# Kernel optimization log

Measured on AMD Instinct MI355X. Metric: run time of the kernel, lower is better.

Reference implementation:

```python
import jax, jax.numpy as jnp
import numpy as np

MAX_COLLISIONS = 8
EPS = 1e-6


def _interval(p, dd):
    """Moller interval on the intersection line. p, dd: [..., 3] projections and
    signed plane distances of one triangle's vertices. Returns (lo, hi)."""
    p0, p1, p2 = p[..., 0], p[..., 1], p[..., 2]
    d0, d1, d2 = dd[..., 0], dd[..., 1], dd[..., 2]

    def seg(pa, da, pb, db, pc, dc):
        # vertex a is isolated on one side of the other triangle's plane
        den1 = db - da
        den2 = dc - da
        den1 = jnp.where(jnp.abs(den1) < 1e-12, 1e-12, den1)
        den2 = jnp.where(jnp.abs(den2) < 1e-12, 1e-12, den2)
        t1 = pb + (pa - pb) * db / den1
        t2 = pc + (pa - pc) * dc / den2
        return jnp.minimum(t1, t2), jnp.maximum(t1, t2)

    lo2, hi2 = seg(p2, d2, p0, d0, p1, d1)  # verts 0,1 on same side -> 2 isolated
    lo1, hi1 = seg(p1, d1, p0, d0, p2, d2)  # verts 0,2 on same side -> 1 isolated
    lo0, hi0 = seg(p0, d0, p1, d1, p2, d2)  # verts 1,2 on same side -> 0 isolated
    c2 = d0 * d1 > 0
    c1 = jnp.logical_and(~c2, d0 * d2 > 0)
    lo = jnp.where(c2, lo2, jnp.where(c1, lo1, lo0))
    hi = jnp.where(c2, hi2, jnp.where(c1, hi1, hi0))
    return lo, hi


def _collide_mask(tris):
    """tris: [B, F, 3, 3]. Returns bool [B, F, F] (upper-triangular) of
    triangle-triangle intersections (Moller test, coplanar pairs ignored,
    pairs sharing a vertex excluded -- same policy as the BVH CUDA kernel)."""
    B, F = tris.shape[0], tris.shape[1]
    v0 = tris[..., 0, :]
    N = jnp.cross(tris[..., 1, :] - v0, tris[..., 2, :] - v0)  # [B,F,3]
    d = -jnp.einsum('bfc,bfc->bf', N, v0)

    # du[b,f,g,k]: signed distance of triangle g's vertex k to plane of triangle f
    du = jnp.einsum('bfc,bgkc->bfgk', N, tris) + d[:, :, None, None]
    # dv[b,f,g,k]: signed distance of triangle f's vertex k to plane of triangle g
    dv = jnp.einsum('bgc,bfkc->bfgk', N, tris) + d[:, None, :, None]
    du = jnp.where(jnp.abs(du) < EPS, 0.0, du)
    dv = jnp.where(jnp.abs(dv) < EPS, 0.0, dv)

    no_u = (du[..., 0] * du[..., 1] > 0) & (du[..., 0] * du[..., 2] > 0)
    no_v = (dv[..., 0] * dv[..., 1] > 0) & (dv[..., 0] * dv[..., 2] > 0)
    coplanar = jnp.all(du == 0.0, axis=-1)

    # direction of the plane-plane intersection line; project onto dominant axis
    D = jnp.cross(N[:, :, None, :], N[:, None, :, :])  # [B,F,F,3]
    axis = jnp.argmax(jnp.abs(D), axis=-1)             # [B,F,F]
    oh = jax.nn.one_hot(axis, 3, dtype=tris.dtype)     # [B,F,F,3]
    vp = jnp.einsum('bfkc,bfgc->bfgk', tris, oh)  # proj of tri f's verts
    up = jnp.einsum('bgkc,bfgc->bfgk', tris, oh)  # proj of tri g's verts

    lo1, hi1 = _interval(vp, dv)
    lo2, hi2 = _interval(up, du)
    overlap = jnp.maximum(lo1, lo2) <= jnp.minimum(hi1, hi2)

    collide = (~no_u) & (~no_v) & (~coplanar) & overlap

    # exclude pairs sharing a vertex (exact coordinate match), and i >= j
    shared = jnp.any(
        jnp.all(tris[:, :, None, :, None, :] == tris[:, None, :, None, :, :], axis=-1),
        axis=(-1, -2))
    upper = jnp.triu(jnp.ones((F, F), dtype=bool), k=1)
    return collide & (~shared) & upper


def setup_inputs() -> dict:
    key = jax.random.key(0)
    triangles = jax.random.normal(key, (2, 1024, 3, 3), dtype=jnp.float32)
    return {"triangles": triangles}


def reference(triangles):
    B, F = triangles.shape[0], triangles.shape[1]
    K = F * MAX_COLLISIONS  # fixed-size output slot count, as in the CUDA kernel
    mask = _collide_mask(triangles)             # [B,F,F] bool
    flat = mask.reshape(B, F * F)
    # stable sort: colliding pairs (True) first, in (i,j) lexicographic order
    order = jnp.argsort(~flat, axis=1)[:, :K]   # [B,K]
    valid = jnp.take_along_axis(flat, order, axis=1)
    pairs = jnp.stack([order // F, order % F], axis=-1)  # [B,K,2]
    pairs = jnp.where(valid[..., None], pairs, -1)
    return pairs.astype(jnp.int32)
```

## Files before the change

### kernel.cpp

```cpp
#include <hip/hip_runtime.h>
#include <hip/hip_bf16.h>

#pragma clang fp contract(off)

#define F 1024
#define MAXC 8
#define K (F * MAXC)
#define WORDS_PER_ROW 16
#define WORDS_PER_BATCH (F * WORDS_PER_ROW)
#define EPS 1e-6f
#define IT 8

#define WS_MASK(ws) ((unsigned long long*)(ws))

__device__ __forceinline__ void tri_plane(const float* T, float N[3], float& d) {
    float e1x = T[3] - T[0], e1y = T[4] - T[1], e1z = T[5] - T[2];
    float e2x = T[6] - T[0], e2y = T[7] - T[1], e2z = T[8] - T[2];
    N[0] = e1y * e2z - e1z * e2y;
    N[1] = e1z * e2x - e1x * e2z;
    N[2] = e1x * e2y - e1y * e2x;
    d = -((N[0] * T[0] + N[1] * T[1]) + N[2] * T[2]);
}

__device__ __forceinline__ void interval_sel(
    float p0, float p1, float p2, float d0, float d1, float d2,
    float& lo, float& hi) {
    bool c2 = (d0 * d1 > 0.0f);
    bool c1 = (!c2) && (d0 * d2 > 0.0f);
    bool c21 = c2 || c1;
    float pa = c2 ? p2 : (c1 ? p1 : p0);
    float da = c2 ? d2 : (c1 ? d1 : d0);
    float pb = c21 ? p0 : p1;
    float db = c21 ? d0 : d1;
    float pc = c2 ? p1 : p2;
    float dc = c2 ? d1 : d2;
    float den1 = db - da;
    float den2 = dc - da;
    if (fabsf(den1) < 1e-12f) den1 = 1e-12f;
    if (fabsf(den2) < 1e-12f) den2 = 1e-12f;
    float t1 = pb + (pa - pb) * db / den1;
    float t2 = pc + (pa - pc) * dc / den2;
    lo = fminf(t1, t2);
    hi = fmaxf(t1, t2);
}

__global__ __launch_bounds__(256) void pairs_kernel(
    const float* __restrict__ tris, unsigned long long* __restrict__ mask) {
    const int b = blockIdx.z;
    const int i0 = blockIdx.y * IT;
    const int j0 = blockIdx.x * 256;
    const int tid = threadIdx.x;
    const float* tb = tris + (size_t)b * F * 9;
    unsigned long long* mb = mask + (size_t)b * WORDS_PER_BATCH;
    const int word0 = j0 >> 6;

    if (j0 + 255 <= i0) {
        if (tid < IT * 4) {
            int r = tid >> 2, w = tid & 3;
            mb[(i0 + r) * WORDS_PER_ROW + word0 + w] = 0ull;
        }
        return;
    }

    __shared__ float sh[256 * 9];
    __shared__ float shPl[IT][4];
    __shared__ float shTf[IT][9];
    {
        const float4* src = (const float4*)(tb + j0 * 9);
        float4* dst = (float4*)sh;
        for (int idx = tid; idx < 576; idx += 256)
            dst[idx] = src[idx];
    }
    if (tid < IT) {
        const float* T = tb + (i0 + tid) * 9;
        float N[3], d;
        tri_plane(T, N, d);
        shPl[tid][0] = N[0]; shPl[tid][1] = N[1];
        shPl[tid][2] = N[2]; shPl[tid][3] = d;
        #pragma unroll
        for (int k = 0; k < 9; k++) shTf[tid][k] = T[k];
    }
    __syncthreads();

    const int j = j0 + tid;
    const int lane = tid & 63;
    const int wv = tid >> 6;
    const int jmax = j0 + (wv << 6) + 63;

    float g0 = sh[tid * 9 + 0], g1 = sh[tid * 9 + 1], g2 = sh[tid * 9 + 2];
    float g3 = sh[tid * 9 + 3], g4 = sh[tid * 9 + 4], g5 = sh[tid * 9 + 5];
    float g6 = sh[tid * 9 + 6], g7 = sh[tid * 9 + 7], g8 = sh[tid * 9 + 8];
    float Ng0, Ng1, Ng2, dg;
    {
        float e1x = g3 - g0, e1y = g4 - g1, e1z = g5 - g2;
        float e2x = g6 - g0, e2y = g7 - g1, e2z = g8 - g2;
        Ng0 = e1y * e2z - e1z * e2y;
        Ng1 = e1z * e2x - e1x * e2z;
        Ng2 = e1x * e2y - e1y * e2x;
        dg = -((Ng0 * g0 + Ng1 * g1) + Ng2 * g2);
    }

    #pragma unroll 1
    for (int r = 0; r < IT; r++) {
        const int i = i0 + r;
        unsigned long long bal = 0ull;
        if (jmax > i) {
            float Nf0 = shPl[r][0], Nf1 = shPl[r][1], Nf2 = shPl[r][2];
            float df = shPl[r][3];
            float f0 = shTf[r][0], f1 = shTf[r][1], f2 = shTf[r][2];
            float f3 = shTf[r][3], f4 = shTf[r][4], f5 = shTf[r][5];
            float f6 = shTf[r][6], f7 = shTf[r][7], f8 = shTf[r][8];

            float x0 = ((Nf0 * g0 + Nf1 * g1) + Nf2 * g2) + df;
            float x1 = ((Nf0 * g3 + Nf1 * g4) + Nf2 * g5) + df;
            float x2 = ((Nf0 * g6 + Nf1 * g7) + Nf2 * g8) + df;
            float du0 = (fabsf(x0) < EPS) ? 0.0f : x0;
            float du1 = (fabsf(x1) < EPS) ? 0.0f : x1;
            float du2 = (fabsf(x2) < EPS) ? 0.0f : x2;
            float y0 = ((Ng0 * f0 + Ng1 * f1) + Ng2 * f2) + dg;
            float y1 = ((Ng0 * f3 + Ng1 * f4) + Ng2 * f5) + dg;
            float y2 = ((Ng0 * f6 + Ng1 * f7) + Ng2 * f8) + dg;
            float dv0 = (fabsf(y0) < EPS) ? 0.0f : y0;
            float dv1 = (fabsf(y1) < EPS) ? 0.0f : y1;
            float dv2 = (fabsf(y2) < EPS) ? 0.0f : y2;

            bool no_u = (du0 * du1 > 0.0f) && (du0 * du2 > 0.0f);
            bool no_v = (dv0 * dv1 > 0.0f) && (dv0 * dv2 > 0.0f);
            bool coplanar = (du0 == 0.0f) && (du1 == 0.0f) && (du2 == 0.0f);

            float D0 = Nf1 * Ng2 - Nf2 * Ng1;
            float D1 = Nf2 * Ng0 - Nf0 * Ng2;
            float D2 = Nf0 * Ng1 - Nf1 * Ng0;
            float a0 = fabsf(D0), a1 = fabsf(D1), a2 = fabsf(D2);
            int axis = 0;
            float m = a0;
            if (a1 > m) { axis = 1; m = a1; }
            if (a2 > m) { axis = 2; }

            float vp0 = (axis == 0) ? f0 : ((axis == 1) ? f1 : f2);
            float vp1 = (axis == 0) ? f3 : ((axis == 1) ? f4 : f5);
            float vp2 = (axis == 0) ? f6 : ((axis == 1) ? f7 : f8);
            float up0 = (axis == 0) ? g0 : ((axis == 1) ? g1 : g2);
            float up1 = (axis == 0) ? g3 : ((axis == 1) ? g4 : g5);
            float up2 = (axis == 0) ? g6 : ((axis == 1) ? g7 : g8);

            float lo1, hi1, lo2, hi2;
            interval_sel(vp0, vp1, vp2, dv0, dv1, dv2, lo1, hi1);
            interval_sel(up0, up1, up2, du0, du1, du2, lo2, hi2);
            bool overlap = fmaxf(lo1, lo2) <= fminf(hi1, hi2);

            bool pred = (j > i) && !no_u && !no_v && !coplanar && overlap;
            bal = __ballot(pred);
        }
        if (lane == 0)
            mb[i * WORDS_PER_ROW + word0 + wv] = bal;
    }
}

__global__ __launch_bounds__(256) void compact_fused(
    const unsigned long long* __restrict__ mask, int* __restrict__ out) {
    const int b = blockIdx.y;
    const int k = blockIdx.x;
    const int tid = threadIdx.x;
    const unsigned long long* m = mask + (size_t)b * WORDS_PER_BATCH;

    unsigned long long myw = 0ull;
    int pref = 0, tot = 0;
    #pragma unroll 8
    for (int c = 0; c < 64; c++) {
        unsigned long long w = m[c * 256 + tid];
        int pc = __popcll(w);
        tot += pc;
        if (c < k) pref += pc;
        if (c == k) myw = w;
    }
    int myc = __popcll(myw);

    const int lane = tid & 63;
    const int wv = tid >> 6;

    int x = myc;
    #pragma unroll
    for (int off = 1; off < 64; off <<= 1) {
        int y = __shfl_up(x, off);
        if (lane >= off) x += y;
    }
    #pragma unroll
    for (int off = 32; off > 0; off >>= 1) {
        pref += __shfl_xor(pref, off);
        tot  += __shfl_xor(tot, off);
    }
    __shared__ int s_wsum[4], s_pref[4], s_tot[4];
    if (lane == 63) s_wsum[wv] = x;
    if (lane == 0) { s_pref[wv] = pref; s_tot[wv] = tot; }
    __syncthreads();
    int base = 0;
    #pragma unroll
    for (int t = 0; t < 4; t++)
        if (t < wv) base += s_wsum[t];
    int prefix = s_pref[0] + s_pref[1] + s_pref[2] + s_pref[3];
    int total  = s_tot[0] + s_tot[1] + s_tot[2] + s_tot[3];

    int rank = prefix + base + (x - myc);
    int* ob = out + (size_t)b * K * 2;

    int word = k * 256 + tid;
    if (word < K && word >= total) {
        ob[word * 2 + 0] = -1;
        ob[word * 2 + 1] = -1;
    }

    int base_flat = word << 6;
    while (myw) {
        int bit = __ffsll((long long)myw) - 1;
        myw &= myw - 1;
        if (rank < K) {
            int flat = base_flat + bit;
            ob[rank * 2 + 0] = flat >> 10;
            ob[rank * 2 + 1] = flat & 1023;
        }
        rank++;
    }
}

extern "C" void kernel_launch(void* const* d_in, const int* in_sizes, int n_in,
                              void* d_out, int out_size, void* d_ws, size_t ws_size,
                              hipStream_t stream) {
    const float* tris = (const float*)d_in[0];
    int* out = (int*)d_out;
    unsigned long long* mask = WS_MASK(d_ws);

    dim3 gridA(F / 256, F / IT, 2);
    pairs_kernel<<<gridA, 256, 0, stream>>>(tris, mask);

    dim3 gridC(64, 2);
    compact_fused<<<gridC, 256, 0, stream>>>(mask, out);
}
```

Measured before the change: 73.74 us.

## Launch only live upper-triangle tiles and mask dead words in compaction

The pair kernel now launches only the tiles that touch the upper triangle, mapping a linear block index to (column, row-tile), so no blocks are spent writing zero words for fully lower-triangular regions. Because those mask words are no longer written, the compaction kernel computes per-thread a row threshold and zeros out any word below the diagonal instead of reading stale workspace. The row loop is also unrolled by two and the mask write moved inside the live branch. The risk is relying on the threshold math to match exactly which words were written, since stale workspace would otherwise corrupt the results.

Result: faster. 72.27 us (-2.0%).

```diff
diff --git a/kernel.cpp b/kernel.cpp
--- a/kernel.cpp
+++ b/kernel.cpp
@@ -1,5 +1,4 @@
 #include <hip/hip_runtime.h>
-#include <hip/hip_bf16.h>
 
 #pragma clang fp contract(off)
 
@@ -10,6 +9,7 @@
 #define WORDS_PER_BATCH (F * WORDS_PER_ROW)
 #define EPS 1e-6f
 #define IT 8
+#define LIVE_TILES 320
 
 #define WS_MASK(ws) ((unsigned long long*)(ws))
 
@@ -46,21 +46,19 @@
 
 __global__ __launch_bounds__(256) void pairs_kernel(
     const float* __restrict__ tris, unsigned long long* __restrict__ mask) {
-    const int b = blockIdx.z;
-    const int i0 = blockIdx.y * IT;
-    const int j0 = blockIdx.x * 256;
+    const int b = blockIdx.y;
+    const int t = blockIdx.x;
+    int c, r;
+    if (t < 32)       { c = 0; r = t; }
+    else if (t < 96)  { c = 1; r = t - 32; }
+    else if (t < 192) { c = 2; r = t - 96; }
+    else              { c = 3; r = t - 192; }
+    const int i0 = r * IT;
+    const int j0 = c * 256;
     const int tid = threadIdx.x;
     const float* tb = tris + (size_t)b * F * 9;
     unsigned long long* mb = mask + (size_t)b * WORDS_PER_BATCH;
     const int word0 = j0 >> 6;
-
-    if (j0 + 255 <= i0) {
-        if (tid < IT * 4) {
-            int r = tid >> 2, w = tid & 3;
-            mb[(i0 + r) * WORDS_PER_ROW + word0 + w] = 0ull;
-        }
-        return;
-    }
 
     __shared__ float sh[256 * 9];
     __shared__ float shPl[IT][4];
@@ -100,16 +98,15 @@
         dg = -((Ng0 * g0 + Ng1 * g1) + Ng2 * g2);
     }
 
-    #pragma unroll 1
-    for (int r = 0; r < IT; r++) {
-        const int i = i0 + r;
-        unsigned long long bal = 0ull;
+    #pragma unroll 2
+    for (int rr = 0; rr < IT; rr++) {
+        const int i = i0 + rr;
         if (jmax > i) {
-            float Nf0 = shPl[r][0], Nf1 = shPl[r][1], Nf2 = shPl[r][2];
-            float df = shPl[r][3];
-            float f0 = shTf[r][0], f1 = shTf[r][1], f2 = shTf[r][2];
-            float f3 = shTf[r][3], f4 = shTf[r][4], f5 = shTf[r][5];
-            float f6 = shTf[r][6], f7 = shTf[r][7], f8 = shTf[r][8];
+            float Nf0 = shPl[rr][0], Nf1 = shPl[rr][1], Nf2 = shPl[rr][2];
+            float df = shPl[rr][3];
+            float f0 = shTf[rr][0], f1 = shTf[rr][1], f2 = shTf[rr][2];
+            float f3 = shTf[rr][3], f4 = shTf[rr][4], f5 = shTf[rr][5];
+            float f6 = shTf[rr][6], f7 = shTf[rr][7], f8 = shTf[rr][8];
 
             float x0 = ((Nf0 * g0 + Nf1 * g1) + Nf2 * g2) + df;
             float x1 = ((Nf0 * g3 + Nf1 * g4) + Nf2 * g5) + df;
@@ -150,10 +147,10 @@
             bool overlap = fmaxf(lo1, lo2) <= fminf(hi1, hi2);
 
             bool pred = (j > i) && !no_u && !no_v && !coplanar && overlap;
-            bal = __ballot(pred);
+            unsigned long long bal = __ballot(pred);
+            if (lane == 0)
+                mb[i * WORDS_PER_ROW + word0 + wv] = bal;
         }
-        if (lane == 0)
-            mb[i * WORDS_PER_ROW + word0 + wv] = bal;
     }
 }
 
@@ -164,11 +161,16 @@
     const int tid = threadIdx.x;
     const unsigned long long* m = mask + (size_t)b * WORDS_PER_BATCH;
 
+    const int jm = (tid & 15) * 64 + 63;
+    const int ih = tid >> 4;
+    const int cthr = (jm - ih + 15) >> 4;
+
     unsigned long long myw = 0ull;
     int pref = 0, tot = 0;
     #pragma unroll 8
     for (int c = 0; c < 64; c++) {
         unsigned long long w = m[c * 256 + tid];
+        w = (c < cthr) ? w : 0ull;
         int pc = __popcll(w);
         tot += pc;
         if (c < k) pref += pc;
@@ -230,7 +232,7 @@
     int* out = (int*)d_out;
     unsigned long long* mask = WS_MASK(d_ws);
 
-    dim3 gridA(F / 256, F / IT, 2);
+    dim3 gridA(LIVE_TILES, 2);
     pairs_kernel<<<gridA, 256, 0, stream>>>(tris, mask);
 
     dim3 gridC(64, 2);
```
